# Optimization experiments

Hardware: AMD Instinct MI355X
Metric: run time of the kernel (lower is better)

## Reference

```python
import jax, jax.numpy as jnp
import numpy as np

N_NODES = 100000
N_EDGES = 1200000
N_GRAPHS = 256
IN_C, HID_C, OUT_C = 5, 64, 2


def gcn_conv(x, src, dst, W, b, n_nodes):
    """PyG GCNConv: h = x@W; add self-loops; deg from target col (edge weight 1);
    norm = deg^{-1/2}[src]*deg^{-1/2}[dst]; scatter-add messages into dst; + bias."""
    loop = jnp.arange(n_nodes, dtype=src.dtype)
    s = jnp.concatenate([src, loop])
    d = jnp.concatenate([dst, loop])
    deg = jax.ops.segment_sum(jnp.ones_like(d, dtype=x.dtype), d, num_segments=n_nodes)
    dinv = jnp.where(deg > 0, jax.lax.rsqrt(deg), 0.0)
    norm = dinv[s] * dinv[d]                     # [E+N]
    h = x @ W                                    # [N, out]
    msg = h[s] * norm[:, None]                   # gather + scale  [E+N, out]
    out = jax.ops.segment_sum(msg, d, num_segments=n_nodes)  # scatter-add
    return out + b


def setup_inputs() -> dict:
    key = jax.random.key(0)
    ks = jax.random.split(key, 10)
    x = jax.random.normal(ks[0], (N_NODES, IN_C), dtype=jnp.float32)
    edge_index = jax.random.randint(ks[1], (2, N_EDGES), 0, N_NODES, dtype=jnp.int64)
    batch = jnp.sort(jax.random.randint(ks[2], (N_NODES,), 0, N_GRAPHS, dtype=jnp.int64))
    def glorot(k, fan_in, fan_out):
        lim = np.sqrt(6.0 / (fan_in + fan_out))
        return jax.random.uniform(k, (fan_in, fan_out), jnp.float32, -lim, lim)
    W1 = glorot(ks[3], IN_C, HID_C)
    b1 = jnp.zeros((HID_C,), jnp.float32)
    W2 = glorot(ks[4], HID_C, HID_C)
    b2 = jnp.zeros((HID_C,), jnp.float32)
    Wfc = glorot(ks[5], HID_C, OUT_C)
    bfc = jnp.zeros((OUT_C,), jnp.float32)
    return {"x": x, "edge_index": edge_index, "batch": batch,
            "W1": W1, "b1": b1, "W2": W2, "b2": b2, "Wfc": Wfc, "bfc": bfc}


def reference(x, edge_index, batch, W1, b1, W2, b2, Wfc, bfc):
    src, dst = edge_index[0], edge_index[1]
    h = jax.nn.relu(gcn_conv(x, src, dst, W1, b1, N_NODES))
    h = jax.nn.relu(gcn_conv(h, src, dst, W2, b2, N_NODES))
    # global_mean_pool over graph ids in `batch`
    sums = jax.ops.segment_sum(h, batch, num_segments=N_GRAPHS)          # [G, H]
    cnts = jax.ops.segment_sum(jnp.ones((h.shape[0],), h.dtype), batch,
                               num_segments=N_GRAPHS)                    # [G]
    pooled = sums / jnp.maximum(cnts, 1.0)[:, None]
    return pooled @ Wfc + bfc                                            # [G, 2]
```

## Files before the change

kernel.cpp:

```cpp
#include <hip/hip_runtime.h>

#define N_NODES 100000
#define N_EDGES 1200000
#define N_GRAPHS 256
#define IN_C 5
#define HID_C 64
#define OUT_C 2

#define BSH 7
#define BNODES 128
#define NB ((N_NODES + BNODES - 1) / BNODES)
#define CAPB 2048
#define EPB 16384
#define NBLK_E ((N_EDGES + EPB - 1) / EPB)
#define GNPW 8
#define L1NPW 8

typedef unsigned int uint32;

__device__ __forceinline__ uint32 f2bf(float f) {
    uint32 x = __float_as_uint(f);
    return (x + 0x7FFFu + ((x >> 16) & 1u)) >> 16;
}
__device__ __forceinline__ float bflo(uint32 r) { return __uint_as_float(r << 16); }
__device__ __forceinline__ float bfhi(uint32 r) { return __uint_as_float(r & 0xFFFF0000u); }

__global__ void k_bscatter(const int* __restrict__ src, const int* __restrict__ dst,
                           int* __restrict__ bcnt, int* __restrict__ pairs,
                           float* __restrict__ pooled) {
    __shared__ int h[NB];
    if (blockIdx.x < (N_GRAPHS * HID_C) / 512)
        pooled[blockIdx.x * 512 + threadIdx.x] = 0.f;
    for (int i = threadIdx.x; i < NB; i += blockDim.x) h[i] = 0;
    __syncthreads();
    int e0 = blockIdx.x * EPB;
    int e1 = e0 + EPB; if (e1 > N_EDGES) e1 = N_EDGES;
    for (int e = e0 + threadIdx.x; e < e1; e += blockDim.x)
        atomicAdd(&h[dst[e] >> BSH], 1);
    __syncthreads();
    for (int i = threadIdx.x; i < NB; i += blockDim.x)
        if (h[i]) h[i] = (i << 11) + atomicAdd(&bcnt[i], h[i]);
    __syncthreads();
    for (int e = e0 + threadIdx.x; e < e1; e += blockDim.x) {
        int d = dst[e];
        int pos = atomicAdd(&h[d >> BSH], 1);
        pairs[pos] = ((d & (BNODES - 1)) << 17) | src[e];
    }
}

__global__ void k_bsort_xs(const int* __restrict__ pairs, const int* __restrict__ bcnt,
                           const float* __restrict__ x,
                           int* __restrict__ csr, int* __restrict__ rs,
                           int* __restrict__ cnt, float* __restrict__ dinv,
                           float* __restrict__ xs) {
    __shared__ int spairs[CAPB];
    __shared__ int ssorted[CAPB];
    __shared__ int hist[BNODES];
    __shared__ int tmp[BNODES];
    __shared__ int cur[BNODES];
    __shared__ float sdv[BNODES];
    int b = blockIdx.x;
    int t = threadIdx.x;
    int base = b << BSH;
    if (t < BNODES) hist[t] = 0;
    __syncthreads();
    int s = b << 11;
    int n = bcnt[b];
    if (n > CAPB) n = CAPB;
    for (int i = t; i < n; i += 256) {
        int p = pairs[s + i];
        spairs[i] = p;
        atomicAdd(&hist[p >> 17], 1);
    }
    __syncthreads();
    int v = (t < BNODES) ? hist[t] : 0;
    if (t < BNODES) tmp[t] = v;
    __syncthreads();
    for (int off = 1; off < BNODES; off <<= 1) {
        int a = (t < BNODES && t >= off) ? tmp[t - off] : 0;
        __syncthreads();
        if (t < BNODES) tmp[t] += a;
        __syncthreads();
    }
    float dv_t = rsqrtf((float)v + 1.0f);
    if (t < BNODES) {
        cur[t] = tmp[t] - v;
        sdv[t] = dv_t;
        if (base + t < N_NODES) {
            rs[base + t] = s + tmp[t] - v;
            cnt[base + t] = v;
            dinv[base + t] = dv_t;
        }
    }
    __syncthreads();
    for (int i = t; i < n; i += 256) {
        int p = spairs[i];
        int pos = atomicAdd(&cur[p >> 17], 1);
        ssorted[pos] = p & 0x1FFFF;
    }
    __syncthreads();
    for (int i = t; i < n; i += 256)
        csr[s + i] = ssorted[i];
    for (int i = t; i < BNODES * 8; i += 256) {
        int nl = i >> 3, k = i & 7;
        int node = base + nl;
        if (node < N_NODES && k < IN_C)
            xs[(unsigned)node * 8 + k] = x[(unsigned)node * IN_C + k] * sdv[nl];
    }
}

__global__ void __launch_bounds__(256) k_l1(
        const float* __restrict__ xs, const int* __restrict__ csr,
        const int* __restrict__ rs, const int* __restrict__ cnt,
        const float* __restrict__ dinv, const float* __restrict__ b1,
        const float* __restrict__ W1, const float* __restrict__ W2,
        uint32* __restrict__ g2t) {
    __shared__ __align__(16) float sagg[4][L1NPW][8];
    __shared__ __align__(16) float srow[4][2][HID_C];
    int tid = threadIdx.x;
    int w = tid >> 6;
    int lane = tid & 63;
    int base = (blockIdx.x * 4 + w) * L1NPW;

    int g = lane >> 3, l = lane & 7;
    int v = base + g;
    float a0 = 0.f, a1 = 0.f, a2 = 0.f, a3 = 0.f, a4 = 0.f;
    if (v < N_NODES) {
        int k0 = rs[v];
        int n = cnt[v];
        if (l == 0) {
            float4 p = *(const float4*)&xs[(unsigned)v * 8];
            a0 = p.x; a1 = p.y; a2 = p.z; a3 = p.w;
            a4 = xs[(unsigned)v * 8 + 4];
        }
        int i = l;
        int un = (i < n) ? csr[k0 + i] : -1;
        while (un >= 0) {
            int u = un;
            i += 8;
            un = (i < n) ? csr[k0 + i] : -1;
            float4 p = *(const float4*)&xs[(unsigned)u * 8];
            float p4 = xs[(unsigned)u * 8 + 4];
            a0 += p.x; a1 += p.y; a2 += p.z; a3 += p.w; a4 += p4;
        }
    }
#pragma unroll
    for (int off = 4; off; off >>= 1) {
        a0 += __shfl_xor(a0, off);
        a1 += __shfl_xor(a1, off);
        a2 += __shfl_xor(a2, off);
        a3 += __shfl_xor(a3, off);
        a4 += __shfl_xor(a4, off);
    }
    if (l == 0 && v < N_NODES) {
        *(float4*)&sagg[w][g][0] = make_float4(a0, a1, a2, a3);
        sagg[w][g][4] = a4;
    }

    int half = lane >> 5, c2 = lane & 31;
    int kb = half << 5;
    float2 w1r[IN_C];
#pragma unroll
    for (int k = 0; k < IN_C; ++k)
        w1r[k] = *(const float2*)&W1[k * HID_C + 2 * c2];
    float2 w2r[32];
#pragma unroll
    for (int j = 0; j < 32; ++j)
        w2r[j] = *(const float2*)&W2[(kb + j) * HID_C + 2 * c2];
    float2 bias = *(const float2*)&b1[2 * c2];

    for (int gg = 0; gg < L1NPW; ++gg) {
        int node = base + gg;
        if (node >= N_NODES) break;
        float dv = dinv[node];
        float4 qa = *(const float4*)&sagg[w][gg][0];
        float q4 = sagg[w][gg][4];
        float s0 = qa.x * w1r[0].x + qa.y * w1r[1].x + qa.z * w1r[2].x
                 + qa.w * w1r[3].x + q4 * w1r[4].x;
        float s1 = qa.x * w1r[0].y + qa.y * w1r[1].y + qa.z * w1r[2].y
                 + qa.w * w1r[3].y + q4 * w1r[4].y;
        float h0 = fmaxf(s0 * dv + bias.x, 0.f);
        float h1 = fmaxf(s1 * dv + bias.y, 0.f);
        int buf = gg & 1;
        if (half == 0) *(float2*)&srow[w][buf][2 * c2] = make_float2(h0, h1);
        float t0 = 0.f, t1 = 0.f;
#pragma unroll
        for (int jj = 0; jj < 8; ++jj) {
            float4 hv = *(const float4*)&srow[w][buf][kb + 4 * jj];
            t0 += hv.x * w2r[4 * jj + 0].x + hv.y * w2r[4 * jj + 1].x
                + hv.z * w2r[4 * jj + 2].x + hv.w * w2r[4 * jj + 3].x;
            t1 += hv.x * w2r[4 * jj + 0].y + hv.y * w2r[4 * jj + 1].y
                + hv.z * w2r[4 * jj + 2].y + hv.w * w2r[4 * jj + 3].y;
        }
        t0 += __shfl_xor(t0, 32);
        t1 += __shfl_xor(t1, 32);
        if (half == 0)
            g2t[(unsigned)node * 32 + c2] = (f2bf(t1 * dv) << 16) | f2bf(t0 * dv);
    }
}

#define LDU2(d, u) uint2 d = *(const uint2*)&g[(unsigned)(u) * 32 + 2 * c4]
#define ACC4(s0, s1, s2, s3, r) { s0 += bflo(r.x); s1 += bfhi(r.x); \
                                  s2 += bflo(r.y); s3 += bfhi(r.y); }
__global__ void __launch_bounds__(256, 4) k_gather2p(
        const uint32* __restrict__ g, const int* __restrict__ csr,
        const int* __restrict__ rs, const int* __restrict__ cnt,
        const float* __restrict__ dinv, const float* __restrict__ b,
        const int* __restrict__ batch, float* __restrict__ pooled) {
    int wv = __builtin_amdgcn_readfirstlane(
        blockIdx.x * (blockDim.x >> 6) + (threadIdx.x >> 6));
    int n0 = wv * GNPW;
    if (n0 >= N_NODES) return;
    int lane = threadIdx.x & 63;
    int sub = lane >> 4;
    int c4 = lane & 15;
    int va = n0 + sub, vb = n0 + 4 + sub;
    int ka = rs[va], na = cnt[va];
    int kb = rs[vb], nb = cnt[vb];
    float dva = dinv[va], dvb = dinv[vb];
    int ga = batch[va], gb = batch[vb];
    float4 bias = *(const float4*)&b[4 * c4];
    LDU2(rsa, va); LDU2(rsb, vb);
    float a0 = bflo(rsa.x), a1 = bfhi(rsa.x), a2 = bflo(rsa.y), a3 = bfhi(rsa.y);
    float y0 = bflo(rsb.x), y1 = bfhi(rsb.x), y2 = bflo(rsb.y), y3 = bfhi(rsb.y);
    int ia = 0, ib = 0;
    while (ia + 7 < na && ib + 7 < nb) {
        int u0 = csr[ka+ia+0], u1 = csr[ka+ia+1], u2 = csr[ka+ia+2], u3 = csr[ka+ia+3];
        int u4 = csr[ka+ia+4], u5 = csr[ka+ia+5], u6 = csr[ka+ia+6], u7 = csr[ka+ia+7];
        int w0 = csr[kb+ib+0], w1 = csr[kb+ib+1], w2 = csr[kb+ib+2], w3 = csr[kb+ib+3];
        int w4 = csr[kb+ib+4], w5 = csr[kb+ib+5], w6 = csr[kb+ib+6], w7 = csr[kb+ib+7];
        LDU2(p0, u0); LDU2(p1, u1); LDU2(p2, u2); LDU2(p3, u3);
        LDU2(p4, u4); LDU2(p5, u5); LDU2(p6, u6); LDU2(p7, u7);
        LDU2(q0, w0); LDU2(q1, w1); LDU2(q2, w2); LDU2(q3, w3);
        LDU2(q4, w4); LDU2(q5, w5); LDU2(q6, w6); LDU2(q7, w7);
        ACC4(a0, a1, a2, a3, p0); ACC4(a0, a1, a2, a3, p1);
        ACC4(a0, a1, a2, a3, p2); ACC4(a0, a1, a2, a3, p3);
        ACC4(a0, a1, a2, a3, p4); ACC4(a0, a1, a2, a3, p5);
        ACC4(a0, a1, a2, a3, p6); ACC4(a0, a1, a2, a3, p7);
        ACC4(y0, y1, y2, y3, q0); ACC4(y0, y1, y2, y3, q1);
        ACC4(y0, y1, y2, y3, q2); ACC4(y0, y1, y2, y3, q3);
        ACC4(y0, y1, y2, y3, q4); ACC4(y0, y1, y2, y3, q5);
        ACC4(y0, y1, y2, y3, q6); ACC4(y0, y1, y2, y3, q7);
        ia += 8; ib += 8;
    }
    while (ia + 7 < na) {
        int u0 = csr[ka+ia+0], u1 = csr[ka+ia+1], u2 = csr[ka+ia+2], u3 = csr[ka+ia+3];
        int u4 = csr[ka+ia+4], u5 = csr[ka+ia+5], u6 = csr[ka+ia+6], u7 = csr[ka+ia+7];
        LDU2(p0, u0); LDU2(p1, u1); LDU2(p2, u2); LDU2(p3, u3);
        LDU2(p4, u4); LDU2(p5, u5); LDU2(p6, u6); LDU2(p7, u7);
        ACC4(a0, a1, a2, a3, p0); ACC4(a0, a1, a2, a3, p1);
        ACC4(a0, a1, a2, a3, p2); ACC4(a0, a1, a2, a3, p3);
        ACC4(a0, a1, a2, a3, p4); ACC4(a0, a1, a2, a3, p5);
        ACC4(a0, a1, a2, a3, p6); ACC4(a0, a1, a2, a3, p7);
        ia += 8;
    }
    while (ib + 7 < nb) {
        int w0 = csr[kb+ib+0], w1 = csr[kb+ib+1], w2 = csr[kb+ib+2], w3 = csr[kb+ib+3];
        int w4 = csr[kb+ib+4], w5 = csr[kb+ib+5], w6 = csr[kb+ib+6], w7 = csr[kb+ib+7];
        LDU2(q0, w0); LDU2(q1, w1); LDU2(q2, w2); LDU2(q3, w3);
        LDU2(q4, w4); LDU2(q5, w5); LDU2(q6, w6); LDU2(q7, w7);
        ACC4(y0, y1, y2, y3, q0); ACC4(y0, y1, y2, y3, q1);
        ACC4(y0, y1, y2, y3, q2); ACC4(y0, y1, y2, y3, q3);
        ACC4(y0, y1, y2, y3, q4); ACC4(y0, y1, y2, y3, q5);
        ACC4(y0, y1, y2, y3, q6); ACC4(y0, y1, y2, y3, q7);
        ib += 8;
    }
    while (ia + 3 < na && ib + 3 < nb) {
        int u0 = csr[ka+ia+0], u1 = csr[ka+ia+1], u2 = csr[ka+ia+2], u3 = csr[ka+ia+3];
        int w0 = csr[kb+ib+0], w1 = csr[kb+ib+1], w2 = csr[kb+ib+2], w3 = csr[kb+ib+3];
        LDU2(p0, u0); LDU2(p1, u1); LDU2(p2, u2); LDU2(p3, u3);
        LDU2(q0, w0); LDU2(q1, w1); LDU2(q2, w2); LDU2(q3, w3);
        ACC4(a0, a1, a2, a3, p0); ACC4(a0, a1, a2, a3, p1);
        ACC4(a0, a1, a2, a3, p2); ACC4(a0, a1, a2, a3, p3);
        ACC4(y0, y1, y2, y3, q0); ACC4(y0, y1, y2, y3, q1);
        ACC4(y0, y1, y2, y3, q2); ACC4(y0, y1, y2, y3, q3);
        ia += 4; ib += 4;
    }
    while (ia + 3 < na) {
        int u0 = csr[ka+ia+0], u1 = csr[ka+ia+1], u2 = csr[ka+ia+2], u3 = csr[ka+ia+3];
        LDU2(p0, u0); LDU2(p1, u1); LDU2(p2, u2); LDU2(p3, u3);
        ACC4(a0, a1, a2, a3, p0); ACC4(a0, a1, a2, a3, p1);
        ACC4(a0, a1, a2, a3, p2); ACC4(a0, a1, a2, a3, p3);
        ia += 4;
    }
    while (ib + 3 < nb) {
        int w0 = csr[kb+ib+0], w1 = csr[kb+ib+1], w2 = csr[kb+ib+2], w3 = csr[kb+ib+3];
        LDU2(q0, w0); LDU2(q1, w1); LDU2(q2, w2); LDU2(q3, w3);
        ACC4(y0, y1, y2, y3, q0); ACC4(y0, y1, y2, y3, q1);
        ACC4(y0, y1, y2, y3, q2); ACC4(y0, y1, y2, y3, q3);
        ib += 4;
    }
    while (ia < na && ib < nb) {
        int u0 = csr[ka + ia], w0 = csr[kb + ib];
        LDU2(p0, u0); LDU2(q0, w0);
        ACC4(a0, a1, a2, a3, p0); ACC4(y0, y1, y2, y3, q0);
        ++ia; ++ib;
    }
    while (ia < na) {
        LDU2(p0, csr[ka + ia]);
        ACC4(a0, a1, a2, a3, p0);
        ++ia;
    }
    while (ib < nb) {
        LDU2(q0, csr[kb + ib]);
        ACC4(y0, y1, y2, y3, q0);
        ++ib;
    }
    float oa0 = fmaxf(a0 * dva + bias.x, 0.f);
    float oa1 = fmaxf(a1 * dva + bias.y, 0.f);
    float oa2 = fmaxf(a2 * dva + bias.z, 0.f);
    float oa3 = fmaxf(a3 * dva + bias.w, 0.f);
    float ob0 = fmaxf(y0 * dvb + bias.x, 0.f);
    float ob1 = fmaxf(y1 * dvb + bias.y, 0.f);
    float ob2 = fmaxf(y2 * dvb + bias.z, 0.f);
    float ob3 = fmaxf(y3 * dvb + bias.w, 0.f);
    int g0 = __builtin_amdgcn_readfirstlane(ga);
    if (__all(ga == g0) && __all(gb == g0)) {
        float f0 = oa0 + ob0, f1 = oa1 + ob1, f2 = oa2 + ob2, f3 = oa3 + ob3;
        f0 += __shfl_xor(f0, 16); f0 += __shfl_xor(f0, 32);
        f1 += __shfl_xor(f1, 16); f1 += __shfl_xor(f1, 32);
        f2 += __shfl_xor(f2, 16); f2 += __shfl_xor(f2, 32);
        f3 += __shfl_xor(f3, 16); f3 += __shfl_xor(f3, 32);
        if (sub == 0) {
            atomicAdd(&pooled[g0 * HID_C + 4 * c4 + 0], f0);
            atomicAdd(&pooled[g0 * HID_C + 4 * c4 + 1], f1);
            atomicAdd(&pooled[g0 * HID_C + 4 * c4 + 2], f2);
            atomicAdd(&pooled[g0 * HID_C + 4 * c4 + 3], f3);
        }
    } else {
        atomicAdd(&pooled[ga * HID_C + 4 * c4 + 0], oa0);
        atomicAdd(&pooled[ga * HID_C + 4 * c4 + 1], oa1);
        atomicAdd(&pooled[ga * HID_C + 4 * c4 + 2], oa2);
        atomicAdd(&pooled[ga * HID_C + 4 * c4 + 3], oa3);
        atomicAdd(&pooled[gb * HID_C + 4 * c4 + 0], ob0);
        atomicAdd(&pooled[gb * HID_C + 4 * c4 + 1], ob1);
        atomicAdd(&pooled[gb * HID_C + 4 * c4 + 2], ob2);
        atomicAdd(&pooled[gb * HID_C + 4 * c4 + 3], ob3);
    }
}

__global__ void k_fc(const float* __restrict__ pooled, const int* __restrict__ batch,
                     const float* __restrict__ Wfc, const float* __restrict__ bfc,
                     float* __restrict__ out) {
    int g = blockIdx.x;
    int c = threadIdx.x;
    int lo = 0, hi = N_NODES;
    while (lo < hi) { int mid = (lo + hi) >> 1; if (batch[mid] < g) lo = mid + 1; else hi = mid; }
    int start = lo;
    hi = N_NODES;
    while (lo < hi) { int mid = (lo + hi) >> 1; if (batch[mid] < g + 1) lo = mid + 1; else hi = mid; }
    int n = lo - start;
    float pv = pooled[g * HID_C + c] / (float)(n > 0 ? n : 1);
    float o0 = pv * Wfc[c * OUT_C + 0];
    float o1 = pv * Wfc[c * OUT_C + 1];
#pragma unroll
    for (int off = 32; off > 0; off >>= 1) {
        o0 += __shfl_down(o0, off);
        o1 += __shfl_down(o1, off);
    }
    if (c == 0) {
        out[g * OUT_C + 0] = o0 + bfc[0];
        out[g * OUT_C + 1] = o1 + bfc[1];
    }
}

extern "C" void kernel_launch(void* const* d_in, const int* in_sizes, int n_in,
                              void* d_out, int out_size, void* d_ws, size_t ws_size,
                              hipStream_t stream) {
    const float* x    = (const float*)d_in[0];
    const int*   ei   = (const int*)d_in[1];
    const int*   src  = ei;
    const int*   dst  = ei + N_EDGES;
    const int*   batch= (const int*)d_in[2];
    const float* W1   = (const float*)d_in[3];
    const float* b1   = (const float*)d_in[4];
    const float* W2   = (const float*)d_in[5];
    const float* b2   = (const float*)d_in[6];
    const float* Wfc  = (const float*)d_in[7];
    const float* bfc  = (const float*)d_in[8];
    float* out = (float*)d_out;

    float*  ws     = (float*)d_ws;
    int*    bcnt   = (int*)ws;
    float*  pooled = ws + 1024;
    float*  dinv   = pooled + 16384;
    int*    cnt    = (int*)(dinv + 100352);
    int*    rs     = cnt + 100352;
    int*    pairs  = rs + 100352;
    int*    csr    = pairs + (NB * CAPB);
    float*  xs     = (float*)(csr + (NB * CAPB));
    uint32* g2tab  = (uint32*)(xs + N_NODES * 8);

    hipMemsetAsync(bcnt, 0, 1024 * sizeof(int), stream);

    k_bscatter<<<NBLK_E, 512, 0, stream>>>(src, dst, bcnt, pairs, pooled);
    k_bsort_xs<<<NB, 256, 0, stream>>>(pairs, bcnt, x, csr, rs, cnt, dinv, xs);

    {
        int blocks = (N_NODES + 4 * L1NPW - 1) / (4 * L1NPW);
        k_l1<<<blocks, 256, 0, stream>>>(xs, csr, rs, cnt, dinv, b1, W1, W2, g2tab);
    }

    {
        int waves = (N_NODES + GNPW - 1) / GNPW;
        int blocks = (waves + 3) / 4;
        k_gather2p<<<blocks, 256, 0, stream>>>(g2tab, csr, rs, cnt, dinv, b2, batch, pooled);
    }

    k_fc<<<N_GRAPHS, 64, 0, stream>>>(pooled, batch, Wfc, bfc, out);
}
```

Baseline: 207.4 us.

## Replace global-atomic bucket scatter with per-chunk local sort and segment gather

```diff
diff --git a/kernel.cpp b/kernel.cpp
--- a/kernel.cpp
+++ b/kernel.cpp
@@ -11,8 +11,9 @@
 #define BNODES 128
 #define NB ((N_NODES + BNODES - 1) / BNODES)
 #define CAPB 2048
-#define EPB 16384
-#define NBLK_E ((N_EDGES + EPB - 1) / EPB)
+#define EPB 2048
+#define NCHUNK ((N_EDGES + EPB - 1) / EPB)
+#define SEGS 784
 #define GNPW 8
 #define L1NPW 8
 
@@ -25,36 +26,73 @@
 __device__ __forceinline__ float bflo(uint32 r) { return __uint_as_float(r << 16); }
 __device__ __forceinline__ float bfhi(uint32 r) { return __uint_as_float(r & 0xFFFF0000u); }
 
-__global__ void k_bscatter(const int* __restrict__ src, const int* __restrict__ dst,
-                           int* __restrict__ bcnt, int* __restrict__ pairs,
-                           float* __restrict__ pooled) {
-    __shared__ int h[NB];
-    if (blockIdx.x < (N_GRAPHS * HID_C) / 512)
-        pooled[blockIdx.x * 512 + threadIdx.x] = 0.f;
-    for (int i = threadIdx.x; i < NB; i += blockDim.x) h[i] = 0;
-    __syncthreads();
-    int e0 = blockIdx.x * EPB;
-    int e1 = e0 + EPB; if (e1 > N_EDGES) e1 = N_EDGES;
-    for (int e = e0 + threadIdx.x; e < e1; e += blockDim.x)
-        atomicAdd(&h[dst[e] >> BSH], 1);
-    __syncthreads();
-    for (int i = threadIdx.x; i < NB; i += blockDim.x)
-        if (h[i]) h[i] = (i << 11) + atomicAdd(&bcnt[i], h[i]);
-    __syncthreads();
-    for (int e = e0 + threadIdx.x; e < e1; e += blockDim.x) {
-        int d = dst[e];
-        int pos = atomicAdd(&h[d >> BSH], 1);
-        pairs[pos] = ((d & (BNODES - 1)) << 17) | src[e];
-    }
-}
-
-__global__ void k_bsort_xs(const int* __restrict__ pairs, const int* __restrict__ bcnt,
+__global__ void k_csort(const int* __restrict__ src, const int* __restrict__ dst,
+                        int* __restrict__ pairs, int* __restrict__ seg,
+                        float* __restrict__ pooled) {
+    __shared__ int sp[EPB];
+    __shared__ int hist[782];
+    __shared__ int st[256];
+    int c = blockIdx.x, t = threadIdx.x;
+    if (c < (N_GRAPHS * HID_C) / 256)
+        pooled[c * 256 + t] = 0.f;
+    for (int i = t; i < 782; i += 256) hist[i] = 0;
+    __syncthreads();
+    int e0 = c * EPB;
+    int n = N_EDGES - e0; if (n > EPB) n = EPB;
+    int pk[8], bk[8];
+#pragma unroll
+    for (int i = 0; i < 8; ++i) {
+        int idx = t + i * 256;
+        if (idx < n) {
+            int d = dst[e0 + idx];
+            bk[i] = d >> BSH;
+            pk[i] = ((d & (BNODES - 1)) << 17) | src[e0 + idx];
+            atomicAdd(&hist[bk[i]], 1);
+        } else bk[i] = -1;
+    }
+    __syncthreads();
+    int i0 = t * 4;
+    int v0 = (i0 + 0 < 782) ? hist[i0 + 0] : 0;
+    int v1 = (i0 + 1 < 782) ? hist[i0 + 1] : 0;
+    int v2 = (i0 + 2 < 782) ? hist[i0 + 2] : 0;
+    int v3 = (i0 + 3 < 782) ? hist[i0 + 3] : 0;
+    st[t] = v0 + v1 + v2 + v3;
+    __syncthreads();
+    for (int off = 1; off < 256; off <<= 1) {
+        int a = (t >= off) ? st[t - off] : 0;
+        __syncthreads();
+        st[t] += a;
+        __syncthreads();
+    }
+    int run = (t > 0) ? st[t - 1] : 0;
+    if (i0 + 0 < 782) { hist[i0 + 0] = run; seg[c * SEGS + i0 + 0] = run; run += v0; }
+    if (i0 + 1 < 782) { hist[i0 + 1] = run; seg[c * SEGS + i0 + 1] = run; run += v1; }
+    if (i0 + 2 < 782) { hist[i0 + 2] = run; seg[c * SEGS + i0 + 2] = run; run += v2; }
+    if (i0 + 3 < 782) { hist[i0 + 3] = run; seg[c * SEGS + i0 + 3] = run; run += v3; }
+    if (t == 0) seg[c * SEGS + 782] = n;
+    __syncthreads();
+#pragma unroll
+    for (int i = 0; i < 8; ++i)
+        if (bk[i] >= 0) {
+            int pos = atomicAdd(&hist[bk[i]], 1);
+            sp[pos] = pk[i];
+        }
+    __syncthreads();
+    for (int i = t; i < n; i += 256)
+        pairs[c * EPB + i] = sp[i];
+}
+
+__global__ void k_bsort_xs(const int* __restrict__ pairs, const int* __restrict__ seg,
                            const float* __restrict__ x,
                            int* __restrict__ csr, int* __restrict__ rs,
                            int* __restrict__ cnt, float* __restrict__ dinv,
                            float* __restrict__ xs) {
     __shared__ int spairs[CAPB];
     __shared__ int ssorted[CAPB];
+    __shared__ int slen[NCHUNK];
+    __shared__ int ssrc[NCHUNK];
+    __shared__ int sdst[NCHUNK];
+    __shared__ int st[256];
     __shared__ int hist[BNODES];
     __shared__ int tmp[BNODES];
     __shared__ int cur[BNODES];
@@ -62,15 +100,44 @@
     int b = blockIdx.x;
     int t = threadIdx.x;
     int base = b << BSH;
+    for (int c = t; c < NCHUNK; c += 256) {
+        int s0 = seg[c * SEGS + b];
+        int s1 = seg[c * SEGS + b + 1];
+        slen[c] = s1 - s0;
+        ssrc[c] = c * EPB + s0;
+    }
     if (t < BNODES) hist[t] = 0;
     __syncthreads();
-    int s = b << 11;
-    int n = bcnt[b];
+    int i0 = t * 4;
+    int v0 = (i0 + 0 < NCHUNK) ? slen[i0 + 0] : 0;
+    int v1 = (i0 + 1 < NCHUNK) ? slen[i0 + 1] : 0;
+    int v2 = (i0 + 2 < NCHUNK) ? slen[i0 + 2] : 0;
+    int v3 = (i0 + 3 < NCHUNK) ? slen[i0 + 3] : 0;
+    st[t] = v0 + v1 + v2 + v3;
+    __syncthreads();
+    for (int off = 1; off < 256; off <<= 1) {
+        int a = (t >= off) ? st[t - off] : 0;
+        __syncthreads();
+        st[t] += a;
+        __syncthreads();
+    }
+    int run = (t > 0) ? st[t - 1] : 0;
+    if (i0 + 0 < NCHUNK) { sdst[i0 + 0] = run; run += v0; }
+    if (i0 + 1 < NCHUNK) { sdst[i0 + 1] = run; run += v1; }
+    if (i0 + 2 < NCHUNK) { sdst[i0 + 2] = run; run += v2; }
+    if (i0 + 3 < NCHUNK) { sdst[i0 + 3] = run; run += v3; }
+    __syncthreads();
+    int n = st[255];
     if (n > CAPB) n = CAPB;
-    for (int i = t; i < n; i += 256) {
-        int p = pairs[s + i];
-        spairs[i] = p;
-        atomicAdd(&hist[p >> 17], 1);
+    for (int c = t; c < NCHUNK; c += 256) {
+        int L = slen[c], gs = ssrc[c], d0 = sdst[c];
+        for (int j = 0; j < L; ++j) {
+            int p = pairs[gs + j];
+            if (d0 + j < CAPB) {
+                spairs[d0 + j] = p;
+                atomicAdd(&hist[p >> 17], 1);
+            }
+        }
     }
     __syncthreads();
     int v = (t < BNODES) ? hist[t] : 0;
@@ -83,6 +150,7 @@
         __syncthreads();
     }
     float dv_t = rsqrtf((float)v + 1.0f);
+    int s = b << 11;
     if (t < BNODES) {
         cur[t] = tmp[t] - v;
         sdv[t] = dv_t;
@@ -381,20 +449,18 @@
     float* out = (float*)d_out;
 
     float*  ws     = (float*)d_ws;
-    int*    bcnt   = (int*)ws;
-    float*  pooled = ws + 1024;
-    float*  dinv   = pooled + 16384;
+    float*  pooled = ws;
+    float*  dinv   = ws + 16384;
     int*    cnt    = (int*)(dinv + 100352);
     int*    rs     = cnt + 100352;
-    int*    pairs  = rs + 100352;
-    int*    csr    = pairs + (NB * CAPB);
-    float*  xs     = (float*)(csr + (NB * CAPB));
+    int*    seg    = rs + 100352;
+    int*    pairs  = seg + NCHUNK * SEGS;
+    int*    csr    = pairs + NCHUNK * EPB;
+    float*  xs     = (float*)(csr + NB * CAPB);
     uint32* g2tab  = (uint32*)(xs + N_NODES * 8);
 
-    hipMemsetAsync(bcnt, 0, 1024 * sizeof(int), stream);
-
-    k_bscatter<<<NBLK_E, 512, 0, stream>>>(src, dst, bcnt, pairs, pooled);
-    k_bsort_xs<<<NB, 256, 0, stream>>>(pairs, bcnt, x, csr, rs, cnt, dinv, xs);
+    k_csort<<<NCHUNK, 256, 0, stream>>>(src, dst, pairs, seg, pooled);
+    k_bsort_xs<<<NB, 256, 0, stream>>>(pairs, seg, x, csr, rs, cnt, dinv, xs);
 
     {
         int blocks = (N_NODES + 4 * L1NPW - 1) / (4 * L1NPW);
```

Result: faster. 190.8 us (-8.0%).
